# Kernel optimization log

Hardware: AMD Instinct MI355X
Metric: run time of the kernel (lower is better)

## Reference

```python
import jax, jax.numpy as jnp
import numpy as np
import math

B, L, D = 4, 1024, 1024
A, H = 1024, 16
DH = A // H  # head_size = 64
SCALE = 1.0 / math.sqrt(D)  # note: module scales by sqrt(input_size), not head_size
LN_EPS = 1e-5


def setup_inputs() -> dict:
    key = jax.random.key(0)
    ks = jax.random.split(key, 10)
    def xavier(k, fan_in, fan_out):
        lim = math.sqrt(6.0 / (fan_in + fan_out))
        return jax.random.uniform(k, (fan_out, fan_in), jnp.float32, -lim, lim)
    return {
        "x": jax.random.normal(ks[0], (B, L, D), jnp.float32),
        "queries": jax.random.normal(ks[1], (B, L, D), jnp.float32),
        "Wk": xavier(ks[2], D, A),
        "Wq_self": xavier(ks[3], D, A),
        "Wq_other": xavier(ks[4], D, A),
        "Wv": xavier(ks[5], D, A),
        "Wo": xavier(ks[6], A, A),
        "bo": jnp.zeros((A,), jnp.float32),
        "gamma": jnp.ones((A,), jnp.float32),
        "beta": jnp.zeros((A,), jnp.float32),
        "attention_mask": jnp.ones((B, L), jnp.int32),
    }


def reference(x, queries, Wk, Wq_self, Wq_other, Wv, Wo, bo, gamma, beta, attention_mask):
    # projections (Linear: y = x @ W.T), split heads to (B, L, H, DH)
    def proj(inp, W):
        return (inp @ W.T).reshape(B, L, H, DH)
    k = proj(x, Wk)
    q_self = proj(x, Wq_self)
    q_other = proj(queries, Wq_other)
    v = proj(x, Wv)

    # scores_self + scores_other == (q_self + q_other) @ k^T  (algebraically identical)
    q_comb = q_self + q_other
    scores = jnp.einsum("bqhd,bkhd->bhqk", q_comb, k) * SCALE  # (B, H, L, L)

    # mask: (B, L) -> (B, 1, 1, L) broadcast over heads and query positions
    m = attention_mask.astype(scores.dtype)[:, None, None, :]
    scores = scores + (1.0 - m) * -100000.0

    attn = jax.nn.softmax(scores, axis=-1)  # dropout p=0 -> identity

    out = jnp.einsum("bhqk,bkhd->bqhd", attn, v).reshape(B, L, A)

    # FF output: Linear -> identity activation -> LayerNorm (dropout=0)
    out = out @ Wo.T + bo
    mu = jnp.mean(out, axis=-1, keepdims=True)
    var = jnp.var(out, axis=-1, keepdims=True)
    out = (out - mu) * jax.lax.rsqrt(var + LN_EPS) * gamma + beta
    return out
```

## Files before the change

kernel.cpp:

```cpp
#include <hip/hip_runtime.h>
#include <hip/hip_bf16.h>
#include <math.h>

#define BB 4
#define LL 1024
#define DD 1024
#define AA 1024
#define HH 16
#define DHH 64
#define LOG2E 1.44269504f
#define QSC 0.045084223f
#define MBIAS -144269.5f

typedef __attribute__((ext_vector_type(8))) short short8;
typedef __attribute__((ext_vector_type(4))) float floatx4;

__device__ __forceinline__ float bf2f(unsigned short u) {
    union { unsigned u; float f; } x; x.u = ((unsigned)u) << 16; return x.f;
}
__device__ __forceinline__ unsigned short f2bf(float f) {
    union { float f; unsigned u; } x; x.f = f;
    unsigned r = x.u + 0x7fffu + ((x.u >> 16) & 1u);
    return (unsigned short)(r >> 16);
}
__device__ __forceinline__ unsigned pkbf(float a, float b) {
    union { __hip_bfloat162 h; unsigned u; } c;
    c.h = __float22bfloat162_rn(make_float2(a, b));
    return c.u;
}

__device__ __forceinline__ void gload16(const void* g, const void* l) {
    __builtin_amdgcn_global_load_lds(
        (const __attribute__((address_space(1))) unsigned int*)g,
        (__attribute__((address_space(3))) unsigned int*)l, 16, 0, 0);
}

__device__ __forceinline__ void remap8(int& bx, int& by) {
    const int lin = blockIdx.x + (blockIdx.y << 4);
    const int xcd = lin & 7, f = lin >> 3;
    by = ((xcd >> 1) << 3) + (f >> 3);
    bx = ((xcd & 1) << 3) + (f & 7);
}

struct ConvDesc { const float* s[12]; unsigned short* d[12]; };

__global__ __launch_bounds__(256) void conv_f2b(ConvDesc cd) {
    const int u  = blockIdx.x >> 10;
    const int lb = blockIdx.x & 1023;
    const int idx = lb * 1024 + threadIdx.x * 4;
    float4 v = *reinterpret_cast<const float4*>(cd.s[u] + idx);
    uint2 o;
    o.x = pkbf(v.x, v.y);
    o.y = pkbf(v.z, v.w);
    *reinterpret_cast<uint2*>(cd.d[u] + idx) = o;
}

template <bool BBF>
__device__ __forceinline__ void gemm_pass(const unsigned short* A, const void* Bv,
                                          int mblk, int nblk,
                                          int kbase, int ksteps,
                                          unsigned short* As, unsigned short* Bs,
                                          floatx4 (&acc)[4][2])
{
    const int tid  = threadIdx.x;
    const int lane = tid & 63;
    const int l16  = lane & 15;
    const int quad = lane >> 4;
    const int wave = tid >> 6;
    const int wm = wave >> 1, wn = wave & 1;
    const int arow = wave * 8 + (lane >> 3);
    const int acol = ((lane & 7) ^ (lane >> 3)) << 3;
    const unsigned short* Bb = (const unsigned short*)Bv;
    const float* Bf = (const float*)Bv;
    const int brow = tid >> 3;
    const int bcol = (tid & 7) << 3;
    const int bslot = ((tid & 7) ^ (brow & 7)) << 3;

    float4 br[4];
    if (!BBF) {
        const float* p0 = Bf + (size_t)(nblk + brow) * DD + kbase + bcol;
        const float* p1 = Bf + (size_t)(nblk + brow + 32) * DD + kbase + bcol;
        br[0] = ((const float4*)p0)[0]; br[1] = ((const float4*)p0)[1];
        br[2] = ((const float4*)p1)[0]; br[3] = ((const float4*)p1)[1];
    }

    for (int s = 0; s < ksteps; ++s) {
        const int k0 = kbase + s * 64;
        __syncthreads();
        for (int is = 0; is < 4; ++is)
            gload16(A + (size_t)(mblk + is * 32 + arow) * DD + k0 + acol,
                    As + is * 2048 + wave * 512);
        if (BBF) {
            for (int is = 0; is < 2; ++is)
                gload16(Bb + (size_t)(nblk + is * 32 + arow) * DD + k0 + acol,
                        Bs + is * 2048 + wave * 512);
        } else {
            uint4 t0, t1;
            t0.x = pkbf(br[0].x, br[0].y); t0.y = pkbf(br[0].z, br[0].w);
            t0.z = pkbf(br[1].x, br[1].y); t0.w = pkbf(br[1].z, br[1].w);
            t1.x = pkbf(br[2].x, br[2].y); t1.y = pkbf(br[2].z, br[2].w);
            t1.z = pkbf(br[3].x, br[3].y); t1.w = pkbf(br[3].z, br[3].w);
            *reinterpret_cast<uint4*>(Bs + brow * 64 + bslot) = t0;
            *reinterpret_cast<uint4*>(Bs + (brow + 32) * 64 + bslot) = t1;
        }
        __syncthreads();
        if (!BBF && s + 1 < ksteps) {
            const int nk = k0 + 64;
            const float* p0 = Bf + (size_t)(nblk + brow) * DD + nk + bcol;
            const float* p1 = Bf + (size_t)(nblk + brow + 32) * DD + nk + bcol;
            br[0] = ((const float4*)p0)[0]; br[1] = ((const float4*)p0)[1];
            br[2] = ((const float4*)p1)[0]; br[3] = ((const float4*)p1)[1];
        }
        for (int kh = 0; kh < 2; ++kh) {
            const int sl = ((kh * 4 + quad) ^ (l16 & 7)) << 3;
            short8 af[4], bfr[2];
            for (int i = 0; i < 4; ++i)
                af[i] = *reinterpret_cast<const short8*>(
                    As + (wm * 64 + i * 16 + l16) * 64 + sl);
            for (int j = 0; j < 2; ++j)
                bfr[j] = *reinterpret_cast<const short8*>(
                    Bs + (wn * 32 + j * 16 + l16) * 64 + sl);
            for (int i = 0; i < 4; ++i)
                for (int j = 0; j < 2; ++j)
                    acc[i][j] = __builtin_amdgcn_mfma_f32_16x16x32_bf16(
                        af[i], bfr[j], acc[i][j], 0, 0, 0);
        }
    }
}

__device__ __forceinline__ void store_nat(floatx4 (&acc)[4][2], unsigned short* As,
                                          unsigned short* C, int mblk, int nblk)
{
    const int lane = threadIdx.x & 63;
    const int l16  = lane & 15;
    const int quad = lane >> 4;
    const int wave = threadIdx.x >> 6;
    const int wm = wave >> 1, wn = wave & 1;
    __syncthreads();
    unsigned short* Cw = As + wave * 2048;
    for (int i = 0; i < 4; ++i)
        for (int j = 0; j < 2; ++j)
            for (int r = 0; r < 4; ++r)
                Cw[(i * 16 + quad * 4 + r) * 32 + j * 16 + l16] = f2bf(acc[i][j][r]);
    __asm__ volatile("s_waitcnt lgkmcnt(0)" ::: "memory");
    const int mb = mblk + wm * 64;
    const int nb = nblk + wn * 32;
    for (int s = 0; s < 4; ++s) {
        const int row = s * 16 + (lane >> 2);
        uint4 v = *reinterpret_cast<const uint4*>(Cw + row * 32 + (lane & 3) * 8);
        *reinterpret_cast<uint4*>(C + (size_t)(mb + row) * AA + nb + (lane & 3) * 8) = v;
    }
}

__device__ __forceinline__ void store_vt(floatx4 (&acc)[4][2], unsigned short* As,
                                         unsigned short* vt, int mblk, int h)
{
    const int lane = threadIdx.x & 63;
    const int l16  = lane & 15;
    const int quad = lane >> 4;
    const int wave = threadIdx.x >> 6;
    const int wm = wave >> 1, wn = wave & 1;
    __syncthreads();
    unsigned short* Cw = As + wave * 2048;
    for (int i = 0; i < 4; ++i)
        for (int j = 0; j < 2; ++j) {
            ushort4 pv;
            pv.x = f2bf(acc[i][j][0]); pv.y = f2bf(acc[i][j][1]);
            pv.z = f2bf(acc[i][j][2]); pv.w = f2bf(acc[i][j][3]);
            *reinterpret_cast<ushort4*>(&Cw[(j * 16 + l16) * 64 + i * 16 + quad * 4]) = pv;
        }
    __asm__ volatile("s_waitcnt lgkmcnt(0)" ::: "memory");
    const int mg = mblk + wm * 64;
    const int b  = mg >> 10, lbase = mg & 1023;
    for (int s = 0; s < 4; ++s) {
        const int drow = s * 8 + (lane >> 3);
        uint4 v = *reinterpret_cast<const uint4*>(Cw + drow * 64 + (lane & 7) * 8);
        *reinterpret_cast<uint4*>(
            vt + (size_t)((b * HH + h) * DHH + wn * 32 + drow) * LL + lbase + (lane & 7) * 8) = v;
    }
}

template <bool BBF>
__global__ __launch_bounds__(256) void gemm_proj3(
    const unsigned short* __restrict__ xb, const unsigned short* __restrict__ qb,
    const void* __restrict__ Wqs, const void* __restrict__ Wqo,
    const void* __restrict__ Wk, const void* __restrict__ Wv,
    unsigned short* __restrict__ qc, unsigned short* __restrict__ kk,
    unsigned short* __restrict__ vt)
{
    __shared__ alignas(16) unsigned short As[128 * 64];
    __shared__ alignas(16) unsigned short Bs[64 * 64];
    floatx4 acc[4][2] = {};
    int bx, by; remap8(bx, by);
    const int mblk = by * 128, nblk = bx * 64;
    if (blockIdx.z == 0) {
        gemm_pass<BBF>(xb, Wqs, mblk, nblk, 0, 16, As, Bs, acc);
        gemm_pass<BBF>(qb, Wqo, mblk, nblk, 0, 16, As, Bs, acc);
        store_nat(acc, As, qc, mblk, nblk);
    } else if (blockIdx.z == 1) {
        gemm_pass<BBF>(xb, Wk, mblk, nblk, 0, 16, As, Bs, acc);
        store_nat(acc, As, kk, mblk, nblk);
    } else {
        gemm_pass<BBF>(xb, Wv, mblk, nblk, 0, 16, As, Bs, acc);
        store_vt(acc, As, vt, mblk, bx);
    }
}

__global__ __launch_bounds__(256) void gemm_projqk(
    const unsigned short* __restrict__ xb, const unsigned short* __restrict__ qb,
    const float* __restrict__ Wqs, const float* __restrict__ Wqo,
    const float* __restrict__ Wk,
    unsigned short* __restrict__ qc, unsigned short* __restrict__ kk)
{
    __shared__ alignas(16) unsigned short As[128 * 64];
    __shared__ alignas(16) unsigned short Bs[64 * 64];
    floatx4 acc[4][2] = {};
    int bx, by; remap8(bx, by);
    const int mblk = by * 128, nblk = bx * 64;
    if (blockIdx.z == 0) {
        gemm_pass<false>(xb, Wqs, mblk, nblk, 0, 16, As, Bs, acc);
        gemm_pass<false>(qb, Wqo, mblk, nblk, 0, 16, As, Bs, acc);
        store_nat(acc, As, qc, mblk, nblk);
    } else {
        gemm_pass<false>(xb, Wk, mblk, nblk, 0, 16, As, Bs, acc);
        store_nat(acc, As, kk, mblk, nblk);
    }
}

__global__ __launch_bounds__(256) void gemm_v(
    const unsigned short* __restrict__ xb, const float* __restrict__ Wv,
    unsigned short* __restrict__ vt)
{
    __shared__ alignas(16) unsigned short As[128 * 64];
    __shared__ alignas(16) unsigned short Bs[64 * 64];
    floatx4 acc[4][2] = {};
    int bx, by; remap8(bx, by);
    gemm_pass<false>(xb, Wv, by * 128, bx * 64, 0, 16, As, Bs, acc);
    store_vt(acc, As, vt, by * 128, bx);
}

template <bool BBF>
__global__ __launch_bounds__(256) void gemm_wo(
    const unsigned short* __restrict__ ao, const void* __restrict__ Wo,
    unsigned short* __restrict__ pj0, unsigned short* __restrict__ pj1)
{
    __shared__ alignas(16) unsigned short As[128 * 64];
    __shared__ alignas(16) unsigned short Bs[64 * 64];
    floatx4 acc[4][2] = {};
    int bx, by; remap8(bx, by);
    const int z = blockIdx.z;
    gemm_pass<BBF>(ao, Wo, by * 128, bx * 64, z * 512, 8, As, Bs, acc);
    store_nat(acc, As, z ? pj1 : pj0, by * 128, bx * 64);
}

__device__ __forceinline__ int swzb(int row, int slot) {
    return (row << 7) + ((slot ^ (row & 7)) << 4);
}

__global__ __launch_bounds__(256, 4) void attn_flash(const unsigned short* qc,
                                                     const unsigned short* __restrict__ kmat,
                                                     const unsigned short* __restrict__ vt,
                                                     const int* __restrict__ mask,
                                                     unsigned short* ao)
{
    const int blk = blockIdx.x;
    const int xcd = blk & 7;
    const int sub = blk >> 3;
    const int bh  = xcd * 8 + (sub >> 4);
    const int qt  = sub & 15;
    const int b   = bh >> 4;
    const int h   = bh & 15;

    const int wave = threadIdx.x >> 6;
    const int lane = threadIdx.x & 63;
    const int l16  = lane & 15;
    const int quad = lane >> 4;
    const int q0 = qt * 64 + wave * 16;

    __shared__ alignas(16) unsigned short Ks[2][64 * 64];
    __shared__ alignas(16) unsigned short Vs[2][64 * 64];
    __shared__ float Ml[LL];

    const int* bm = mask + b * LL;
    for (int i = 0; i < 4; ++i) {
        const int c = threadIdx.x + i * 256;
        Ml[c] = (1.0f - (float)bm[c]) * MBIAS;
    }

    short8 aq[2];
    for (int s = 0; s < 2; ++s) {
        const unsigned short* p =
            qc + (size_t)(b * LL + q0 + l16) * AA + h * DHH + s * 32 + quad * 8;
        short8 t = *reinterpret_cast<const short8*>(p);
        for (int e = 0; e < 8; ++e)
            t[e] = (short)f2bf(bf2f((unsigned short)t[e]) * QSC);
        aq[s] = t;
    }

    floatx4 O[4] = {};
    float lp = 0.f;

    const unsigned short* kbase = kmat + (size_t)(b * LL) * AA + h * DHH;
    const unsigned short* vbase = vt + (size_t)((b * HH + h) * DHH) * LL;
    const int c0 = threadIdx.x, c1 = threadIdx.x + 256;
    const int row0 = c0 >> 3, slot0 = c0 & 7;
    const int row1 = c1 >> 3, slot1 = c1 & 7;

    uint4 kr0, kr1, vr0, vr1;
    kr0 = *reinterpret_cast<const uint4*>(kbase + (size_t)row0 * AA + slot0 * 8);
    kr1 = *reinterpret_cast<const uint4*>(kbase + (size_t)row1 * AA + slot1 * 8);
    vr0 = *reinterpret_cast<const uint4*>(vbase + (size_t)row0 * LL + slot0 * 8);
    vr1 = *reinterpret_cast<const uint4*>(vbase + (size_t)row1 * LL + slot1 * 8);
    *reinterpret_cast<uint4*>((char*)Ks[0] + swzb(row0, slot0)) = kr0;
    *reinterpret_cast<uint4*>((char*)Ks[0] + swzb(row1, slot1)) = kr1;
    *reinterpret_cast<uint4*>((char*)Vs[0] + swzb(row0, slot0)) = vr0;
    *reinterpret_cast<uint4*>((char*)Vs[0] + swzb(row1, slot1)) = vr1;
    {
        const unsigned short* kb1 = kbase + (size_t)64 * AA;
        const unsigned short* vb1 = vbase + 64;
        kr0 = *reinterpret_cast<const uint4*>(kb1 + (size_t)row0 * AA + slot0 * 8);
        kr1 = *reinterpret_cast<const uint4*>(kb1 + (size_t)row1 * AA + slot1 * 8);
        vr0 = *reinterpret_cast<const uint4*>(vb1 + (size_t)row0 * LL + slot0 * 8);
        vr1 = *reinterpret_cast<const uint4*>(vb1 + (size_t)row1 * LL + slot1 * 8);
    }
    __syncthreads();

    const int srcA = ((quad & 1) << 5) + l16;
    const int srcB = srcA + 16;
    const bool hi = quad >= 2;
    int cur = 0;

    for (int t = 0; t < 16; ++t) {
        const char* Kc = (const char*)Ks[cur];
        const char* Vc = (const char*)Vs[cur];
        if (t + 1 < 16) {
            char* Kn = (char*)Ks[cur ^ 1];
            char* Vn = (char*)Vs[cur ^ 1];
            *reinterpret_cast<uint4*>(Kn + swzb(row0, slot0)) = kr0;
            *reinterpret_cast<uint4*>(Kn + swzb(row1, slot1)) = kr1;
            *reinterpret_cast<uint4*>(Vn + swzb(row0, slot0)) = vr0;
            *reinterpret_cast<uint4*>(Vn + swzb(row1, slot1)) = vr1;
        }
        if (t + 2 < 16) {
            const unsigned short* kb2 = kbase + (size_t)(t + 2) * 64 * AA;
            const unsigned short* vb2 = vbase + (t + 2) * 64;
            kr0 = *reinterpret_cast<const uint4*>(kb2 + (size_t)row0 * AA + slot0 * 8);
            kr1 = *reinterpret_cast<const uint4*>(kb2 + (size_t)row1 * AA + slot1 * 8);
            vr0 = *reinterpret_cast<const uint4*>(vb2 + (size_t)row0 * LL + slot0 * 8);
            vr1 = *reinterpret_cast<const uint4*>(vb2 + (size_t)row1 * LL + slot1 * 8);
        }

        floatx4 p[4];
        const float* Mlb = Ml + t * 64 + quad * 4;
        for (int j = 0; j < 4; ++j) {
            const int rr = j * 16 + l16;
            const short8 kf0 = *reinterpret_cast<const short8*>(Kc + swzb(rr, quad));
            const short8 kf1 = *reinterpret_cast<const short8*>(Kc + swzb(rr, quad + 4));
            floatx4 s_ = {0.f, 0.f, 0.f, 0.f};
            s_ = __builtin_amdgcn_mfma_f32_16x16x32_bf16(kf0, aq[0], s_, 0, 0, 0);
            s_ = __builtin_amdgcn_mfma_f32_16x16x32_bf16(kf1, aq[1], s_, 0, 0, 0);
            const float4 mv = *reinterpret_cast<const float4*>(Mlb + j * 16);
            p[j][0] = exp2f(s_[0] + mv.x);
            p[j][1] = exp2f(s_[1] + mv.y);
            p[j][2] = exp2f(s_[2] + mv.z);
            p[j][3] = exp2f(s_[3] + mv.w);
            lp += (p[j][0] + p[j][1]) + (p[j][2] + p[j][3]);
        }
        unsigned pk[4][2];
        for (int j = 0; j < 4; ++j) {
            pk[j][0] = pkbf(p[j][0], p[j][1]);
            pk[j][1] = pkbf(p[j][2], p[j][3]);
        }
        union { unsigned u[4]; short8 s; } ap0, ap1;
        {
            unsigned xA0 = __shfl((int)pk[0][0], srcA), yA0 = __shfl((int)pk[1][0], srcA);
            unsigned xA1 = __shfl((int)pk[0][1], srcA), yA1 = __shfl((int)pk[1][1], srcA);
            unsigned xB0 = __shfl((int)pk[0][0], srcB), yB0 = __shfl((int)pk[1][0], srcB);
            unsigned xB1 = __shfl((int)pk[0][1], srcB), yB1 = __shfl((int)pk[1][1], srcB);
            ap0.u[0] = hi ? yA0 : xA0;
            ap0.u[1] = hi ? yA1 : xA1;
            ap0.u[2] = hi ? yB0 : xB0;
            ap0.u[3] = hi ? yB1 : xB1;
        }
        {
            unsigned xA0 = __shfl((int)pk[2][0], srcA), yA0 = __shfl((int)pk[3][0], srcA);
            unsigned xA1 = __shfl((int)pk[2][1], srcA), yA1 = __shfl((int)pk[3][1], srcA);
            unsigned xB0 = __shfl((int)pk[2][0], srcB), yB0 = __shfl((int)pk[3][0], srcB);
            unsigned xB1 = __shfl((int)pk[2][1], srcB), yB1 = __shfl((int)pk[3][1], srcB);
            ap1.u[0] = hi ? yA0 : xA0;
            ap1.u[1] = hi ? yA1 : xA1;
            ap1.u[2] = hi ? yB0 : xB0;
            ap1.u[3] = hi ? yB1 : xB1;
        }
        for (int t4 = 0; t4 < 4; ++t4) {
            const int rr = t4 * 16 + l16;
            const short8 bv0 = *reinterpret_cast<const short8*>(Vc + swzb(rr, quad));
            const short8 bv1 = *reinterpret_cast<const short8*>(Vc + swzb(rr, quad + 4));
            O[t4] = __builtin_amdgcn_mfma_f32_16x16x32_bf16(ap0.s, bv0, O[t4], 0, 0, 0);
            O[t4] = __builtin_amdgcn_mfma_f32_16x16x32_bf16(ap1.s, bv1, O[t4], 0, 0, 0);
        }
        __syncthreads();
        cur ^= 1;
    }

    lp += __shfl_xor(lp, 16);
    lp += __shfl_xor(lp, 32);
    float linv[4];
    for (int r = 0; r < 4; ++r) {
        const float s = __shfl(lp, quad * 4 + r);
        linv[r] = 1.0f / s;
    }
    for (int t4 = 0; t4 < 4; ++t4)
        for (int r = 0; r < 4; ++r)
            ao[(size_t)(b * LL + q0 + quad * 4 + r) * AA + h * DHH + t4 * 16 + l16] =
                f2bf(O[t4][r] * linv[r]);
}

__global__ __launch_bounds__(256) void ln_f32(const unsigned short* __restrict__ X0,
                                              const unsigned short* __restrict__ X1,
                                              const float* __restrict__ bo,
                                              const float* __restrict__ gamma,
                                              const float* __restrict__ beta,
                                              float* __restrict__ out)
{
    const int row = blockIdx.x;
    const unsigned short* x0 = X0 + (size_t)row * AA;
    const unsigned short* x1 = X1 + (size_t)row * AA;
    float v[4];
    float s = 0.f, s2 = 0.f;
    for (int e = 0; e < 4; ++e) {
        const int c = threadIdx.x + e * 256;
        const float f = bf2f(x0[c]) + bf2f(x1[c]) + bo[c];
        v[e] = f; s += f; s2 += f * f;
    }
    for (int d = 1; d < 64; d <<= 1) { s += __shfl_xor(s, d); s2 += __shfl_xor(s2, d); }
    __shared__ float red[4][2];
    const int wave = threadIdx.x >> 6;
    const int lane = threadIdx.x & 63;
    if (lane == 0) { red[wave][0] = s; red[wave][1] = s2; }
    __syncthreads();
    s  = red[0][0] + red[1][0] + red[2][0] + red[3][0];
    s2 = red[0][1] + red[1][1] + red[2][1] + red[3][1];
    const float mean = s * (1.0f / AA);
    const float var  = s2 * (1.0f / AA) - mean * mean;
    const float rstd = rsqrtf(var + 1e-5f);
    for (int e = 0; e < 4; ++e) {
        const int c = threadIdx.x + e * 256;
        out[(size_t)row * AA + c] = (v[e] - mean) * rstd * gamma[c] + beta[c];
    }
}

extern "C" void kernel_launch(void* const* d_in, const int* in_sizes, int n_in,
                              void* d_out, int out_size, void* d_ws, size_t ws_size,
                              hipStream_t stream)
{
    const float* x     = (const float*)d_in[0];
    const float* qrs   = (const float*)d_in[1];
    const float* Wk    = (const float*)d_in[2];
    const float* Wqs   = (const float*)d_in[3];
    const float* Wqo   = (const float*)d_in[4];
    const float* Wv    = (const float*)d_in[5];
    const float* Wo    = (const float*)d_in[6];
    const float* bo    = (const float*)d_in[7];
    const float* gamma = (const float*)d_in[8];
    const float* beta  = (const float*)d_in[9];
    const int*   mask  = (const int*)d_in[10];

    char* ws = (char*)d_ws;
    unsigned short* xb = (unsigned short*)(ws + (size_t)0);
    unsigned short* qb = (unsigned short*)(ws + ((size_t)8 << 20));
    const bool big  = ws_size >= ((size_t)24 << 20);
    const bool ws32 = ws_size >= ((size_t)32 << 20);
    unsigned short* vt = big ? (unsigned short*)(ws + ((size_t)16 << 20)) : qb;
    unsigned short* Wb = (unsigned short*)(ws + ((size_t)24 << 20));
    unsigned short* Wqs_b = Wb;
    unsigned short* Wqo_b = Wb + (1u << 20);
    unsigned short* Wk_b  = Wb + (2u << 20);
    unsigned short* Wv_b  = Wb + (3u << 20);
    unsigned short* Wo_b  = qb;
    unsigned short* qc = (unsigned short*)d_out;
    unsigned short* kk = (unsigned short*)((char*)d_out + ((size_t)8 << 20));
    unsigned short* ao  = qc;
    unsigned short* pj0 = xb;
    unsigned short* pj1 = ws32 ? vt : kk;

    dim3 gp(AA / 64, (BB * LL) / 128, 3);
    dim3 gw(AA / 64, (BB * LL) / 128, 2);

    if (ws32) {
        ConvDesc cd;
        int nu = 0;
        for (int i = 0; i < 4; ++i) {
            cd.s[nu] = x   + (size_t)i * (1u << 20); cd.d[nu] = xb + (size_t)i * (1u << 20); ++nu;
            cd.s[nu] = qrs + (size_t)i * (1u << 20); cd.d[nu] = qb + (size_t)i * (1u << 20); ++nu;
        }
        cd.s[nu] = Wqs; cd.d[nu] = Wqs_b; ++nu;
        cd.s[nu] = Wqo; cd.d[nu] = Wqo_b; ++nu;
        cd.s[nu] = Wk;  cd.d[nu] = Wk_b;  ++nu;
        cd.s[nu] = Wv;  cd.d[nu] = Wv_b;  ++nu;
        conv_f2b<<<nu * 1024, 256, 0, stream>>>(cd);

        gemm_proj3<true><<<gp, 256, 0, stream>>>(xb, qb, Wqs_b, Wqo_b, Wk_b, Wv_b,
                                                 qc, kk, vt);
        ConvDesc cw;
        cw.s[0] = Wo; cw.d[0] = Wo_b;
        conv_f2b<<<1024, 256, 0, stream>>>(cw);

        attn_flash<<<BB * HH * (LL / 64), 256, 0, stream>>>(qc, kk, vt, mask, ao);
        gemm_wo<true><<<gw, 256, 0, stream>>>(ao, Wo_b, pj0, pj1);
    } else {
        ConvDesc cd;
        for (int i = 0; i < 4; ++i) {
            cd.s[i]     = x   + (size_t)i * (1u << 20); cd.d[i]     = xb + (size_t)i * (1u << 20);
            cd.s[i + 4] = qrs + (size_t)i * (1u << 20); cd.d[i + 4] = qb + (size_t)i * (1u << 20);
        }
        conv_f2b<<<8 * 1024, 256, 0, stream>>>(cd);
        if (big) {
            gemm_proj3<false><<<gp, 256, 0, stream>>>(xb, qb, Wqs, Wqo, Wk, Wv,
                                                      qc, kk, vt);
        } else {
            dim3 g2(AA / 64, (BB * LL) / 128, 2);
            dim3 g1(AA / 64, (BB * LL) / 128);
            gemm_projqk<<<g2, 256, 0, stream>>>(xb, qb, Wqs, Wqo, Wk, qc, kk);
            gemm_v<<<g1, 256, 0, stream>>>(xb, Wv, vt);
        }
        attn_flash<<<BB * HH * (LL / 64), 256, 0, stream>>>(qc, kk, vt, mask, ao);
        gemm_wo<false><<<gw, 256, 0, stream>>>(ao, Wo, pj0, pj1);
    }
    ln_f32<<<BB * LL, 256, 0, stream>>>(pj0, pj1, bo, gamma, beta, (float*)d_out);
}
```

Measured before the change: 217.8 us.

## Split attention over key halves and merge partial outputs in a combine kernel

Replaces the single flash-attention launch with a split-KV version. Each block processes half of the key sequence and writes unnormalized bf16 partial outputs plus row-sum partials into reused workspace buffers. A new combine kernel then adds the two halves and normalizes. The aim is to double the block count and allow higher occupancy (launch bounds 8). The cost is an extra kernel launch, extra global memory traffic for the partial outputs, and bf16 rounding of the unnormalized partials.

```diff
diff --git a/kernel.cpp b/kernel.cpp
--- a/kernel.cpp
+++ b/kernel.cpp
@@ -257,6 +257,176 @@
     return (row << 7) + ((slot ^ (row & 7)) << 4);
 }
 
+__global__ __launch_bounds__(256, 8) void attn_split(
+    const unsigned short* qc,
+    const unsigned short* __restrict__ kmat,
+    const unsigned short* __restrict__ vt,
+    const int* __restrict__ mask,
+    unsigned short* __restrict__ o0, unsigned short* __restrict__ o1,
+    float* __restrict__ lp0, float* __restrict__ lp1)
+{
+    const int blk = blockIdx.x;
+    const int xcd  = blk & 7;
+    const int sub  = blk >> 3;
+    const int bh   = xcd * 8 + (sub >> 5);
+    const int rest = sub & 31;
+    const int qt   = rest >> 1;
+    const int half = rest & 1;
+    const int b = bh >> 4;
+    const int h = bh & 15;
+
+    const int wave = threadIdx.x >> 6;
+    const int lane = threadIdx.x & 63;
+    const int l16  = lane & 15;
+    const int quad = lane >> 4;
+    const int q0 = qt * 64 + wave * 16;
+
+    __shared__ alignas(16) unsigned short Ks[64 * 64];
+    __shared__ alignas(16) unsigned short Vs[64 * 64];
+    __shared__ float Ml[LL];
+
+    const int* bm = mask + b * LL;
+    for (int i = 0; i < 4; ++i) {
+        const int c = threadIdx.x + i * 256;
+        Ml[c] = (1.0f - (float)bm[c]) * MBIAS;
+    }
+
+    short8 aq[2];
+    for (int s = 0; s < 2; ++s) {
+        const unsigned short* p =
+            qc + (size_t)(b * LL + q0 + l16) * AA + h * DHH + s * 32 + quad * 8;
+        short8 t = *reinterpret_cast<const short8*>(p);
+        for (int e = 0; e < 8; ++e)
+            t[e] = (short)f2bf(bf2f((unsigned short)t[e]) * QSC);
+        aq[s] = t;
+    }
+
+    floatx4 O[4] = {};
+    float lp = 0.f;
+
+    const unsigned short* kbase = kmat + (size_t)(b * LL) * AA + h * DHH;
+    const unsigned short* vbase = vt + (size_t)((b * HH + h) * DHH) * LL;
+    const int c0 = threadIdx.x, c1 = threadIdx.x + 256;
+    const int row0 = c0 >> 3, slot0 = c0 & 7;
+    const int row1 = c1 >> 3, slot1 = c1 & 7;
+
+    const int tb = half * 8;
+    uint4 kr0, kr1, vr0, vr1;
+    {
+        const unsigned short* kb0 = kbase + (size_t)tb * 64 * AA;
+        const unsigned short* vb0 = vbase + tb * 64;
+        kr0 = *reinterpret_cast<const uint4*>(kb0 + (size_t)row0 * AA + slot0 * 8);
+        kr1 = *reinterpret_cast<const uint4*>(kb0 + (size_t)row1 * AA + slot1 * 8);
+        vr0 = *reinterpret_cast<const uint4*>(vb0 + (size_t)row0 * LL + slot0 * 8);
+        vr1 = *reinterpret_cast<const uint4*>(vb0 + (size_t)row1 * LL + slot1 * 8);
+    }
+
+    const int srcA = ((quad & 1) << 5) + l16;
+    const int srcB = srcA + 16;
+    const bool hi = quad >= 2;
+
+    for (int tt = 0; tt < 8; ++tt) {
+        const int t = tb + tt;
+        __syncthreads();
+        *reinterpret_cast<uint4*>((char*)Ks + swzb(row0, slot0)) = kr0;
+        *reinterpret_cast<uint4*>((char*)Ks + swzb(row1, slot1)) = kr1;
+        *reinterpret_cast<uint4*>((char*)Vs + swzb(row0, slot0)) = vr0;
+        *reinterpret_cast<uint4*>((char*)Vs + swzb(row1, slot1)) = vr1;
+        __syncthreads();
+        if (tt + 1 < 8) {
+            const unsigned short* kb2 = kbase + (size_t)(t + 1) * 64 * AA;
+            const unsigned short* vb2 = vbase + (t + 1) * 64;
+            kr0 = *reinterpret_cast<const uint4*>(kb2 + (size_t)row0 * AA + slot0 * 8);
+            kr1 = *reinterpret_cast<const uint4*>(kb2 + (size_t)row1 * AA + slot1 * 8);
+            vr0 = *reinterpret_cast<const uint4*>(vb2 + (size_t)row0 * LL + slot0 * 8);
+            vr1 = *reinterpret_cast<const uint4*>(vb2 + (size_t)row1 * LL + slot1 * 8);
+        }
+
+        floatx4 p[4];
+        const float* Mlb = Ml + t * 64 + quad * 4;
+        for (int j = 0; j < 4; ++j) {
+            const int rr = j * 16 + l16;
+            const short8 kf0 = *reinterpret_cast<const short8*>((char*)Ks + swzb(rr, quad));
+            const short8 kf1 = *reinterpret_cast<const short8*>((char*)Ks + swzb(rr, quad + 4));
+            floatx4 s_ = {0.f, 0.f, 0.f, 0.f};
+            s_ = __builtin_amdgcn_mfma_f32_16x16x32_bf16(kf0, aq[0], s_, 0, 0, 0);
+            s_ = __builtin_amdgcn_mfma_f32_16x16x32_bf16(kf1, aq[1], s_, 0, 0, 0);
+            const float4 mv = *reinterpret_cast<const float4*>(Mlb + j * 16);
+            p[j][0] = exp2f(s_[0] + mv.x);
+            p[j][1] = exp2f(s_[1] + mv.y);
+            p[j][2] = exp2f(s_[2] + mv.z);
+            p[j][3] = exp2f(s_[3] + mv.w);
+            lp += (p[j][0] + p[j][1]) + (p[j][2] + p[j][3]);
+        }
+        unsigned pk[4][2];
+        for (int j = 0; j < 4; ++j) {
+            pk[j][0] = pkbf(p[j][0], p[j][1]);
+            pk[j][1] = pkbf(p[j][2], p[j][3]);
+        }
+        union { unsigned u[4]; short8 s; } ap0, ap1;
+        {
+            unsigned xA0 = __shfl((int)pk[0][0], srcA), yA0 = __shfl((int)pk[1][0], srcA);
+            unsigned xA1 = __shfl((int)pk[0][1], srcA), yA1 = __shfl((int)pk[1][1], srcA);
+            unsigned xB0 = __shfl((int)pk[0][0], srcB), yB0 = __shfl((int)pk[1][0], srcB);
+            unsigned xB1 = __shfl((int)pk[0][1], srcB), yB1 = __shfl((int)pk[1][1], srcB);
+            ap0.u[0] = hi ? yA0 : xA0;
+            ap0.u[1] = hi ? yA1 : xA1;
+            ap0.u[2] = hi ? yB0 : xB0;
+            ap0.u[3] = hi ? yB1 : xB1;
+        }
+        {
+            unsigned xA0 = __shfl((int)pk[2][0], srcA), yA0 = __shfl((int)pk[3][0], srcA);
+            unsigned xA1 = __shfl((int)pk[2][1], srcA), yA1 = __shfl((int)pk[3][1], srcA);
+            unsigned xB0 = __shfl((int)pk[2][0], srcB), yB0 = __shfl((int)pk[3][0], srcB);
+            unsigned xB1 = __shfl((int)pk[2][1], srcB), yB1 = __shfl((int)pk[3][1], srcB);
+            ap1.u[0] = hi ? yA0 : xA0;
+            ap1.u[1] = hi ? yA1 : xA1;
+            ap1.u[2] = hi ? yB0 : xB0;
+            ap1.u[3] = hi ? yB1 : xB1;
+        }
+        for (int t4 = 0; t4 < 4; ++t4) {
+            const int rr = t4 * 16 + l16;
+            const short8 bv0 = *reinterpret_cast<const short8*>((char*)Vs + swzb(rr, quad));
+            const short8 bv1 = *reinterpret_cast<const short8*>((char*)Vs + swzb(rr, quad + 4));
+            O[t4] = __builtin_amdgcn_mfma_f32_16x16x32_bf16(ap0.s, bv0, O[t4], 0, 0, 0);
+            O[t4] = __builtin_amdgcn_mfma_f32_16x16x32_bf16(ap1.s, bv1, O[t4], 0, 0, 0);
+        }
+    }
+
+    lp += __shfl_xor(lp, 16);
+    lp += __shfl_xor(lp, 32);
+    unsigned short* op = half ? o1 : o0;
+    float* lpp = half ? lp1 : lp0;
+    if (lane < 16)
+        lpp[(size_t)(b * HH + h) * LL + q0 + lane] = lp;
+    for (int t4 = 0; t4 < 4; ++t4)
+        for (int r = 0; r < 4; ++r)
+            op[(size_t)(b * LL + q0 + quad * 4 + r) * AA + h * DHH + t4 * 16 + l16] =
+                f2bf(O[t4][r]);
+}
+
+__global__ __launch_bounds__(256) void attn_combine(
+    const unsigned short* __restrict__ o0, const unsigned short* __restrict__ o1,
+    const float* __restrict__ lp0, const float* __restrict__ lp1,
+    unsigned short* __restrict__ ao)
+{
+    const int row = blockIdx.x;
+    const int b = row >> 10, l = row & 1023;
+    const int c = threadIdx.x * 4;
+    const int h = c >> 6;
+    const size_t li = (size_t)(b * HH + h) * LL + l;
+    const float linv = 1.0f / (lp0[li] + lp1[li]);
+    const size_t idx = (size_t)row * AA + c;
+    ushort4 a = *reinterpret_cast<const ushort4*>(o0 + idx);
+    ushort4 d = *reinterpret_cast<const ushort4*>(o1 + idx);
+    ushort4 o;
+    o.x = f2bf((bf2f(a.x) + bf2f(d.x)) * linv);
+    o.y = f2bf((bf2f(a.y) + bf2f(d.y)) * linv);
+    o.z = f2bf((bf2f(a.z) + bf2f(d.z)) * linv);
+    o.w = f2bf((bf2f(a.w) + bf2f(d.w)) * linv);
+    *reinterpret_cast<ushort4*>(ao + idx) = o;
+}
+
 __global__ __launch_bounds__(256, 4) void attn_flash(const unsigned short* qc,
                                                      const unsigned short* __restrict__ kmat,
                                                      const unsigned short* __restrict__ vt,
@@ -478,6 +648,10 @@
     unsigned short* Wk_b  = Wb + (2u << 20);
     unsigned short* Wv_b  = Wb + (3u << 20);
     unsigned short* Wo_b  = qb;
+    float* lp0 = (float*)(ws + ((size_t)10 << 20));
+    float* lp1 = (float*)(ws + ((size_t)10 << 20) + ((size_t)512 << 10));
+    unsigned short* o0 = xb;
+    unsigned short* o1 = Wb;
     unsigned short* qc = (unsigned short*)d_out;
     unsigned short* kk = (unsigned short*)((char*)d_out + ((size_t)8 << 20));
     unsigned short* ao  = qc;
@@ -506,7 +680,9 @@
         cw.s[0] = Wo; cw.d[0] = Wo_b;
         conv_f2b<<<1024, 256, 0, stream>>>(cw);
 
-        attn_flash<<<BB * HH * (LL / 64), 256, 0, stream>>>(qc, kk, vt, mask, ao);
+        attn_split<<<BB * HH * (LL / 64) * 2, 256, 0, stream>>>(
+            qc, kk, vt, mask, o0, o1, lp0, lp1);
+        attn_combine<<<BB * LL, 256, 0, stream>>>(o0, o1, lp0, lp1, ao);
         gemm_wo<true><<<gw, 256, 0, stream>>>(ao, Wo_b, pj0, pj1);
     } else {
         ConvDesc cd;
```

New measurement: 269.3 us. +23.6%, slower.
